# Performance work log

Hardware: AMD Instinct MI355X
Metric: run time of the kernel (lower is better)

## Reference

```python
import jax, jax.numpy as jnp
import numpy as np

TOP_K = 8
NUM_EXPERTS = 64


def setup_inputs() -> dict:
    key = jax.random.key(0)
    k1, k2 = jax.random.split(key)
    x = jax.random.normal(k1, (4, 4096, 2048), dtype=jnp.float32)
    # nn.Linear weight [num_experts, d_model], scaled like typical init
    gate_w = jax.random.normal(k2, (NUM_EXPERTS, 2048), dtype=jnp.float32) * 0.02
    expert_bias = jnp.zeros((NUM_EXPERTS,), dtype=jnp.float32)
    return {"x": x, "gate_w": gate_w, "expert_bias": expert_bias}


def reference(x, gate_w, expert_bias):
    # logits = gate(x): [b, s, E]
    logits = jnp.einsum("bsd,ed->bse", x, gate_w)
    # bias is detached in the original (routing-only, no grad)
    logits_with_bias = logits + jax.lax.stop_gradient(expert_bias)
    # top-k over experts
    top_k_logits, top_k_indices = jax.lax.top_k(logits_with_bias, TOP_K)
    # softmax over the small top-k dimension
    top_k_scores = jax.nn.softmax(top_k_logits, axis=-1)
    # scatter-add load counts per expert (training branch)
    flat_indices = top_k_indices.reshape(-1)
    expert_counts = jnp.zeros((NUM_EXPERTS,), dtype=jnp.int32).at[flat_indices].add(1)
    return top_k_scores, top_k_indices, expert_counts
```

## Files before the change

### kernel.cpp

```cpp
#include <hip/hip_runtime.h>
#include <math.h>

#define DIM   2048
#define NEXP  64
#define TOPK  8
#define BM    32
#define NT    512
#define NBLK  512
#define RSTRIDE 260
#define BUF1  (32 * RSTRIDE)

typedef __attribute__((ext_vector_type(8)))  short bf16x8;
typedef __attribute__((ext_vector_type(16))) float f32x16;

#define MFMA(A, B, C) __builtin_amdgcn_mfma_f32_32x32x16_bf16(A, B, C, 0, 0, 0)
#define AS_BF(v) (*(const bf16x8*)&(v))

#define STR2(x) #x
#define STR(x) STR2(x)
#define GL16(dst, p, off) \
    asm volatile("global_load_dwordx4 %0, %1, off offset:" STR(off) \
                 : "=v"(dst) : "v"(p) : "memory")

__device__ inline unsigned int bfpack(float a, float b) {
    unsigned int ua = __float_as_uint(a), ub = __float_as_uint(b);
    unsigned int lo = (ua + 0x7FFFu + ((ua >> 16) & 1u)) >> 16;
    unsigned int hi = (ub + 0x7FFFu + ((ub >> 16) & 1u)) & 0xFFFF0000u;
    return hi | lo;
}
__device__ inline void split2pair(float a, float b, unsigned int& h, unsigned int& m) {
    h = bfpack(a, b);
    float ra = a - __uint_as_float(h << 16);
    float rb = b - __uint_as_float(h & 0xFFFF0000u);
    m = bfpack(ra, rb);
}

__global__ __launch_bounds__(256) void prep_kernel(const float* __restrict__ w,
                                                   unsigned int* __restrict__ wpack) {
    const int u = blockIdx.x * 256 + threadIdx.x;
    const int e = u >> 8, k8 = u & 255;
    const float4 v0 = *(const float4*)(w + (size_t)e * DIM + k8 * 8);
    const float4 v1 = *(const float4*)(w + (size_t)e * DIM + k8 * 8 + 4);
    unsigned int h[4], m[4];
    split2pair(v0.x, v0.y, h[0], m[0]);
    split2pair(v0.z, v0.w, h[1], m[1]);
    split2pair(v1.x, v1.y, h[2], m[2]);
    split2pair(v1.z, v1.w, h[3], m[3]);
    const int wv = k8 >> 5, t = (k8 >> 1) & 15, kh = k8 & 1;
    const int eh = e >> 5, le = e & 31;
    char* base = (char*)wpack + (size_t)wv * 65536 + t * 4096
               + (eh * 2) * 1024 + (kh * 32 + le) * 16;
    *(uint4*)(base)        = (uint4){h[0], h[1], h[2], h[3]};
    *(uint4*)(base + 1024) = (uint4){m[0], m[1], m[2], m[3]};
}

__global__ __launch_bounds__(NT, 4) void router_kernel(
    const float* __restrict__ x,
    const unsigned int* __restrict__ wpack,
    const float* __restrict__ bias,
    float* __restrict__ out,
    int* __restrict__ histws,
    int M)
{
    __shared__ __align__(16) char smem[67584 + 256];
    float* smemf = (float*)smem;
    int* hist = (int*)(smem + 67584);

    const int tid  = threadIdx.x;
    const int bid  = blockIdx.x;
    const int swz  = (bid & 7) * (NBLK / 8) + (bid >> 3);
    const int row0 = swz * BM;
    if (tid < NEXP) hist[tid] = 0;

    const int wv   = tid >> 6;
    const int lane = tid & 63;
    const int lr   = lane & 31;
    const int kh   = lane >> 5;

    const int xr0 = 4 * wv;
    const float* xsrc0 = x + (size_t)(row0 + xr0 + 0) * DIM + lane * 4;
    const float* xsrc1 = x + (size_t)(row0 + xr0 + 1) * DIM + lane * 4;
    const float* xsrc2 = x + (size_t)(row0 + xr0 + 2) * DIM + lane * 4;
    const float* xsrc3 = x + (size_t)(row0 + xr0 + 3) * DIM + lane * 4;
    const int xo0 = (xr0 + 0) * RSTRIDE + (lane << 2);
    const int xo1 = (xr0 + 1) * RSTRIDE + (lane << 2);
    const int xo2 = (xr0 + 2) * RSTRIDE + (lane << 2);
    const int xo3 = (xr0 + 3) * RSTRIDE + (lane << 2);

    const char* wbase = (const char*)wpack + (2 * wv) * 4096 + lane * 16;

    const int g00 = 8 * wv + 2 * kh;
    const int a00 = lr * RSTRIDE + g00 * 4;
    const int a10 = a00 + 16;

    f32x16 acc0 = {}, acc1 = {};
    uint4 xr0_, xr1_, xr2_, xr3_;
    uint4 w0h_, w0m_, w0H_, w0M_, w1h_, w1m_, w1H_, w1M_;

#define XLD(PH) do { \
        GL16(xr0_, xsrc0 + (PH) * 256, 0); \
        GL16(xr1_, xsrc1 + (PH) * 256, 0); \
        GL16(xr2_, xsrc2 + (PH) * 256, 0); \
        GL16(xr3_, xsrc3 + (PH) * 256, 0); \
    } while (0)

#define WLD(PH) do { \
        const char* a_ = wbase + (PH) * 65536; \
        const char* b_ = a_ + 4096; \
        GL16(w0h_, a_, 0);    GL16(w0m_, a_, 1024); \
        GL16(w0H_, a_, 2048); GL16(w0M_, a_, 3072); \
        GL16(w1h_, b_, 0);    GL16(w1m_, b_, 1024); \
        GL16(w1H_, b_, 2048); GL16(w1M_, b_, 3072); \
    } while (0)

#define DSW(BUFO) do { \
        *(uint4*)(smemf + (BUFO) + xo0) = xr0_; \
        *(uint4*)(smemf + (BUFO) + xo1) = xr1_; \
        *(uint4*)(smemf + (BUFO) + xo2) = xr2_; \
        *(uint4*)(smemf + (BUFO) + xo3) = xr3_; \
    } while (0)

#define DOSPLIT(vlo, vhi, hv, mv) do { \
        unsigned int h_[4], m_[4]; \
        split2pair((vlo).x, (vlo).y, h_[0], m_[0]); \
        split2pair((vlo).z, (vlo).w, h_[1], m_[1]); \
        split2pair((vhi).x, (vhi).y, h_[2], m_[2]); \
        split2pair((vhi).z, (vhi).w, h_[3], m_[3]); \
        hv = (uint4){h_[0], h_[1], h_[2], h_[3]}; \
        mv = (uint4){m_[0], m_[1], m_[2], m_[3]}; \
    } while (0)

#define COMPUTE(BUFO) do { \
        float4 alo0_ = *(const float4*)(smemf + (BUFO) + a00); \
        float4 ahi0_ = *(const float4*)(smemf + (BUFO) + a00 + 4); \
        float4 alo1_ = *(const float4*)(smemf + (BUFO) + a10); \
        float4 ahi1_ = *(const float4*)(smemf + (BUFO) + a10 + 4); \
        uint4 ah_, am_; \
        DOSPLIT(alo0_, ahi0_, ah_, am_); \
        acc0 = MFMA(AS_BF(ah_), AS_BF(w0h_), acc0); \
        acc0 = MFMA(AS_BF(am_), AS_BF(w0h_), acc0); \
        acc0 = MFMA(AS_BF(ah_), AS_BF(w0m_), acc0); \
        acc1 = MFMA(AS_BF(ah_), AS_BF(w0H_), acc1); \
        acc1 = MFMA(AS_BF(am_), AS_BF(w0H_), acc1); \
        acc1 = MFMA(AS_BF(ah_), AS_BF(w0M_), acc1); \
        DOSPLIT(alo1_, ahi1_, ah_, am_); \
        acc0 = MFMA(AS_BF(ah_), AS_BF(w1h_), acc0); \
        acc0 = MFMA(AS_BF(am_), AS_BF(w1h_), acc0); \
        acc0 = MFMA(AS_BF(ah_), AS_BF(w1m_), acc0); \
        acc1 = MFMA(AS_BF(ah_), AS_BF(w1H_), acc1); \
        acc1 = MFMA(AS_BF(am_), AS_BF(w1H_), acc1); \
        acc1 = MFMA(AS_BF(ah_), AS_BF(w1M_), acc1); \
    } while (0)

#define VMW(N) do { asm volatile("s_waitcnt vmcnt(" STR(N) ")" ::: "memory"); \
                    __builtin_amdgcn_sched_barrier(0); } while (0)
#define LGK0 asm volatile("s_waitcnt lgkmcnt(0)" ::: "memory")
#define BAR __builtin_amdgcn_s_barrier()

    XLD(0); WLD(0);
    VMW(8);
    DSW(0); LGK0; BAR;

    XLD(1); VMW(4); COMPUTE(0);    WLD(1); VMW(8); DSW(BUF1); LGK0; BAR;
    XLD(2); VMW(4); COMPUTE(BUF1); WLD(2); VMW(8); DSW(0);    LGK0; BAR;
    XLD(3); VMW(4); COMPUTE(0);    WLD(3); VMW(8); DSW(BUF1); LGK0; BAR;
    XLD(4); VMW(4); COMPUTE(BUF1); WLD(4); VMW(8); DSW(0);    LGK0; BAR;
    XLD(5); VMW(4); COMPUTE(0);    WLD(5); VMW(8); DSW(BUF1); LGK0; BAR;
    XLD(6); VMW(4); COMPUTE(BUF1); WLD(6); VMW(8); DSW(0);    LGK0; BAR;
    XLD(7); VMW(4); COMPUTE(0);    WLD(7); VMW(8); DSW(BUF1); LGK0; BAR;
    VMW(0); COMPUTE(BUF1);

#undef VMW
#undef LGK0
#undef COMPUTE
#undef DOSPLIT
#undef DSW
#undef WLD
#undef XLD

    __syncthreads();

    float* lgf = smemf;
    #pragma unroll
    for (int r = 0; r < 16; ++r) {
        const int rr = (r & 3) + 8 * (r >> 2) + 4 * kh;
        lgf[(wv * 32 + rr) * 66 + lr]      = acc0[r];
        lgf[(wv * 32 + rr) * 66 + 32 + lr] = acc1[r];
    }
    __syncthreads();

    float* out_scores = out;
    float* out_idx    = out + (size_t)M * TOPK;

    #pragma unroll
    for (int i = 0; i < 4; ++i) {
        const int row = wv * 4 + i;
        float vm = bias[lane];
        #pragma unroll
        for (int p = 0; p < 8; ++p) vm += lgf[(p * 32 + row) * 66 + lane];

        float vals[TOPK];
        int   ids[TOPK];
        #pragma unroll
        for (int k = 0; k < TOPK; ++k) {
            float mv = vm;
            int   mi = lane;
            #pragma unroll
            for (int off = 32; off > 0; off >>= 1) {
                float ov = __shfl_xor(mv, off);
                int   oi = __shfl_xor(mi, off);
                if (ov > mv || (ov == mv && oi < mi)) { mv = ov; mi = oi; }
            }
            vals[k] = mv; ids[k] = mi;
            if (lane == mi) { vm = -INFINITY; atomicAdd(&hist[mi], 1); }
        }
        if (lane == 0) {
            const float m = vals[0];
            float e[TOPK];
            float ssum = 0.f;
            #pragma unroll
            for (int k = 0; k < TOPK; ++k) { e[k] = expf(vals[k] - m); ssum += e[k]; }
            const float inv = 1.0f / ssum;
            const size_t base = (size_t)(row0 + row) * TOPK;
            #pragma unroll
            for (int k = 0; k < TOPK; ++k) {
                out_scores[base + k] = e[k] * inv;
                out_idx[base + k]    = (float)ids[k];
            }
        }
    }

    __syncthreads();
    if (tid < NEXP) histws[bid * NEXP + tid] = hist[tid];
}

__global__ __launch_bounds__(512) void reduce_kernel(const int* __restrict__ histws,
                                                     float* __restrict__ counts) {
    __shared__ int partl[8][NEXP];
    const int t = threadIdx.x;
    const int e = t & 63, c = t >> 6;
    int sm = 0;
    for (int b = c; b < NBLK; b += 8) sm += histws[b * NEXP + e];
    partl[c][e] = sm;
    __syncthreads();
    if (t < NEXP) {
        int tot = 0;
        #pragma unroll
        for (int i = 0; i < 8; ++i) tot += partl[i][t];
        counts[t] = (float)tot;
    }
}

extern "C" void kernel_launch(void* const* d_in, const int* in_sizes, int n_in,
                              void* d_out, int out_size, void* d_ws, size_t ws_size,
                              hipStream_t stream) {
    const float* x    = (const float*)d_in[0];
    const float* w    = (const float*)d_in[1];
    const float* bias = (const float*)d_in[2];
    float* out = (float*)d_out;
    const int M = in_sizes[0] / DIM;

    unsigned int* wpack = (unsigned int*)d_ws;
    int* histws = (int*)((char*)d_ws + (1u << 20));
    float* out_counts = out + (size_t)2 * M * TOPK;

    prep_kernel<<<64, 256, 0, stream>>>(w, wpack);
    router_kernel<<<NBLK, NT, 0, stream>>>(x, wpack, bias, out, histws, M);
    reduce_kernel<<<1, 512, 0, stream>>>(histws, out_counts);
}
```

Baseline: 69.02 us.

## Double row tile to 64 per block and serialize cross-wave logit reduction

Each block now handles 64 rows instead of 32, with half as many blocks. Each wave covers a K slice for both 32-row halves, so every weight fragment loaded from global feeds two MFMA accumulators, halving weight traffic per row. The K phase is narrowed to 128 so the staging buffers fit, at the cost of twice as many pipeline phases and barriers. The per-wave partial logits are now summed through shared memory in eight sequential steps with a barrier after each, which adds serialization and keeps fewer blocks per CU busy.

```diff
diff --git a/kernel.cpp b/kernel.cpp
--- a/kernel.cpp
+++ b/kernel.cpp
@@ -4,11 +4,11 @@
 #define DIM   2048
 #define NEXP  64
 #define TOPK  8
-#define BM    32
+#define BM    64
 #define NT    512
-#define NBLK  512
-#define RSTRIDE 260
-#define BUF1  (32 * RSTRIDE)
+#define NBLK  256
+#define RSTRIDE 132
+#define BUF1  (BM * RSTRIDE)
 
 typedef __attribute__((ext_vector_type(8)))  short bf16x8;
 typedef __attribute__((ext_vector_type(16))) float f32x16;
@@ -77,40 +77,37 @@
     const int lr   = lane & 31;
     const int kh   = lane >> 5;
 
-    const int xr0 = 4 * wv;
-    const float* xsrc0 = x + (size_t)(row0 + xr0 + 0) * DIM + lane * 4;
-    const float* xsrc1 = x + (size_t)(row0 + xr0 + 1) * DIM + lane * 4;
-    const float* xsrc2 = x + (size_t)(row0 + xr0 + 2) * DIM + lane * 4;
-    const float* xsrc3 = x + (size_t)(row0 + xr0 + 3) * DIM + lane * 4;
-    const int xo0 = (xr0 + 0) * RSTRIDE + (lane << 2);
-    const int xo1 = (xr0 + 1) * RSTRIDE + (lane << 2);
-    const int xo2 = (xr0 + 2) * RSTRIDE + (lane << 2);
-    const int xo3 = (xr0 + 3) * RSTRIDE + (lane << 2);
-
-    const char* wbase = (const char*)wpack + (2 * wv) * 4096 + lane * 16;
-
-    const int g00 = 8 * wv + 2 * kh;
-    const int a00 = lr * RSTRIDE + g00 * 4;
-    const int a10 = a00 + 16;
-
-    f32x16 acc0 = {}, acc1 = {};
+    const int l5  = lane >> 5;
+    const int xr0 = 8 * wv;
+    const float* xsrc0 = x + (size_t)(row0 + xr0 + 0 + l5) * DIM + lr * 4;
+    const float* xsrc1 = x + (size_t)(row0 + xr0 + 2 + l5) * DIM + lr * 4;
+    const float* xsrc2 = x + (size_t)(row0 + xr0 + 4 + l5) * DIM + lr * 4;
+    const float* xsrc3 = x + (size_t)(row0 + xr0 + 6 + l5) * DIM + lr * 4;
+    const int xo0 = (xr0 + 0 + l5) * RSTRIDE + lr * 4;
+    const int xo1 = (xr0 + 2 + l5) * RSTRIDE + lr * 4;
+    const int xo2 = (xr0 + 4 + l5) * RSTRIDE + lr * 4;
+    const int xo3 = (xr0 + 6 + l5) * RSTRIDE + lr * 4;
+
+    const char* wtb = (const char*)wpack + wv * 4096 + lane * 16;
+
+    const int a0 = lr * RSTRIDE + wv * 16 + kh * 8;
+    const int a1 = (32 + lr) * RSTRIDE + wv * 16 + kh * 8;
+
+    f32x16 acc00 = {}, acc01 = {}, acc10 = {}, acc11 = {};
     uint4 xr0_, xr1_, xr2_, xr3_;
-    uint4 w0h_, w0m_, w0H_, w0M_, w1h_, w1m_, w1H_, w1M_;
+    uint4 w0h_, w0m_, w1h_, w1m_;
 
 #define XLD(PH) do { \
-        GL16(xr0_, xsrc0 + (PH) * 256, 0); \
-        GL16(xr1_, xsrc1 + (PH) * 256, 0); \
-        GL16(xr2_, xsrc2 + (PH) * 256, 0); \
-        GL16(xr3_, xsrc3 + (PH) * 256, 0); \
+        GL16(xr0_, xsrc0 + (PH) * 128, 0); \
+        GL16(xr1_, xsrc1 + (PH) * 128, 0); \
+        GL16(xr2_, xsrc2 + (PH) * 128, 0); \
+        GL16(xr3_, xsrc3 + (PH) * 128, 0); \
     } while (0)
 
 #define WLD(PH) do { \
-        const char* a_ = wbase + (PH) * 65536; \
-        const char* b_ = a_ + 4096; \
-        GL16(w0h_, a_, 0);    GL16(w0m_, a_, 1024); \
-        GL16(w0H_, a_, 2048); GL16(w0M_, a_, 3072); \
-        GL16(w1h_, b_, 0);    GL16(w1m_, b_, 1024); \
-        GL16(w1H_, b_, 2048); GL16(w1M_, b_, 3072); \
+        const char* p_ = wtb + ((PH) >> 1) * 65536 + ((PH) & 1) * 32768; \
+        GL16(w0h_, p_, 0);    GL16(w0m_, p_, 1024); \
+        GL16(w1h_, p_, 2048); GL16(w1m_, p_, 3072); \
     } while (0)
 
 #define DSW(BUFO) do { \
@@ -131,25 +128,25 @@
     } while (0)
 
 #define COMPUTE(BUFO) do { \
-        float4 alo0_ = *(const float4*)(smemf + (BUFO) + a00); \
-        float4 ahi0_ = *(const float4*)(smemf + (BUFO) + a00 + 4); \
-        float4 alo1_ = *(const float4*)(smemf + (BUFO) + a10); \
-        float4 ahi1_ = *(const float4*)(smemf + (BUFO) + a10 + 4); \
+        float4 alo0_ = *(const float4*)(smemf + (BUFO) + a0); \
+        float4 ahi0_ = *(const float4*)(smemf + (BUFO) + a0 + 4); \
+        float4 alo1_ = *(const float4*)(smemf + (BUFO) + a1); \
+        float4 ahi1_ = *(const float4*)(smemf + (BUFO) + a1 + 4); \
         uint4 ah_, am_; \
         DOSPLIT(alo0_, ahi0_, ah_, am_); \
-        acc0 = MFMA(AS_BF(ah_), AS_BF(w0h_), acc0); \
-        acc0 = MFMA(AS_BF(am_), AS_BF(w0h_), acc0); \
-        acc0 = MFMA(AS_BF(ah_), AS_BF(w0m_), acc0); \
-        acc1 = MFMA(AS_BF(ah_), AS_BF(w0H_), acc1); \
-        acc1 = MFMA(AS_BF(am_), AS_BF(w0H_), acc1); \
-        acc1 = MFMA(AS_BF(ah_), AS_BF(w0M_), acc1); \
+        acc00 = MFMA(AS_BF(ah_), AS_BF(w0h_), acc00); \
+        acc00 = MFMA(AS_BF(am_), AS_BF(w0h_), acc00); \
+        acc00 = MFMA(AS_BF(ah_), AS_BF(w0m_), acc00); \
+        acc01 = MFMA(AS_BF(ah_), AS_BF(w1h_), acc01); \
+        acc01 = MFMA(AS_BF(am_), AS_BF(w1h_), acc01); \
+        acc01 = MFMA(AS_BF(ah_), AS_BF(w1m_), acc01); \
         DOSPLIT(alo1_, ahi1_, ah_, am_); \
-        acc0 = MFMA(AS_BF(ah_), AS_BF(w1h_), acc0); \
-        acc0 = MFMA(AS_BF(am_), AS_BF(w1h_), acc0); \
-        acc0 = MFMA(AS_BF(ah_), AS_BF(w1m_), acc0); \
-        acc1 = MFMA(AS_BF(ah_), AS_BF(w1H_), acc1); \
-        acc1 = MFMA(AS_BF(am_), AS_BF(w1H_), acc1); \
-        acc1 = MFMA(AS_BF(ah_), AS_BF(w1M_), acc1); \
+        acc10 = MFMA(AS_BF(ah_), AS_BF(w0h_), acc10); \
+        acc10 = MFMA(AS_BF(am_), AS_BF(w0h_), acc10); \
+        acc10 = MFMA(AS_BF(ah_), AS_BF(w0m_), acc10); \
+        acc11 = MFMA(AS_BF(ah_), AS_BF(w1h_), acc11); \
+        acc11 = MFMA(AS_BF(am_), AS_BF(w1h_), acc11); \
+        acc11 = MFMA(AS_BF(ah_), AS_BF(w1m_), acc11); \
     } while (0)
 
 #define VMW(N) do { asm volatile("s_waitcnt vmcnt(" STR(N) ")" ::: "memory"); \
@@ -157,19 +154,33 @@
 #define LGK0 asm volatile("s_waitcnt lgkmcnt(0)" ::: "memory")
 #define BAR __builtin_amdgcn_s_barrier()
 
+#define PHASE(P, BUFC, BUFN) do { \
+        XLD((P) + 1); VMW(4); COMPUTE(BUFC); WLD((P) + 1); VMW(4); \
+        DSW(BUFN); LGK0; BAR; \
+    } while (0)
+
     XLD(0); WLD(0);
-    VMW(8);
+    VMW(4);
     DSW(0); LGK0; BAR;
 
-    XLD(1); VMW(4); COMPUTE(0);    WLD(1); VMW(8); DSW(BUF1); LGK0; BAR;
-    XLD(2); VMW(4); COMPUTE(BUF1); WLD(2); VMW(8); DSW(0);    LGK0; BAR;
-    XLD(3); VMW(4); COMPUTE(0);    WLD(3); VMW(8); DSW(BUF1); LGK0; BAR;
-    XLD(4); VMW(4); COMPUTE(BUF1); WLD(4); VMW(8); DSW(0);    LGK0; BAR;
-    XLD(5); VMW(4); COMPUTE(0);    WLD(5); VMW(8); DSW(BUF1); LGK0; BAR;
-    XLD(6); VMW(4); COMPUTE(BUF1); WLD(6); VMW(8); DSW(0);    LGK0; BAR;
-    XLD(7); VMW(4); COMPUTE(0);    WLD(7); VMW(8); DSW(BUF1); LGK0; BAR;
+    PHASE( 0, 0,    BUF1);
+    PHASE( 1, BUF1, 0);
+    PHASE( 2, 0,    BUF1);
+    PHASE( 3, BUF1, 0);
+    PHASE( 4, 0,    BUF1);
+    PHASE( 5, BUF1, 0);
+    PHASE( 6, 0,    BUF1);
+    PHASE( 7, BUF1, 0);
+    PHASE( 8, 0,    BUF1);
+    PHASE( 9, BUF1, 0);
+    PHASE(10, 0,    BUF1);
+    PHASE(11, BUF1, 0);
+    PHASE(12, 0,    BUF1);
+    PHASE(13, BUF1, 0);
+    PHASE(14, 0,    BUF1);
     VMW(0); COMPUTE(BUF1);
 
+#undef PHASE
 #undef VMW
 #undef LGK0
 #undef COMPUTE
@@ -180,25 +191,34 @@
 
     __syncthreads();
 
-    float* lgf = smemf;
-    #pragma unroll
-    for (int r = 0; r < 16; ++r) {
-        const int rr = (r & 3) + 8 * (r >> 2) + 4 * kh;
-        lgf[(wv * 32 + rr) * 66 + lr]      = acc0[r];
-        lgf[(wv * 32 + rr) * 66 + 32 + lr] = acc1[r];
+    float* lg = smemf;
+    for (int p = 0; p < 8; ++p) {
+        if (wv == p) {
+            #pragma unroll
+            for (int r = 0; r < 16; ++r) {
+                const int rr = (r & 3) + 8 * (r >> 2) + 4 * kh;
+                if (p == 0) {
+                    lg[rr * 66 + lr]             = acc00[r];
+                    lg[rr * 66 + 32 + lr]        = acc01[r];
+                    lg[(32 + rr) * 66 + lr]      = acc10[r];
+                    lg[(32 + rr) * 66 + 32 + lr] = acc11[r];
+                } else {
+                    lg[rr * 66 + lr]             += acc00[r];
+                    lg[rr * 66 + 32 + lr]        += acc01[r];
+                    lg[(32 + rr) * 66 + lr]      += acc10[r];
+                    lg[(32 + rr) * 66 + 32 + lr] += acc11[r];
+                }
+            }
+        }
+        __syncthreads();
     }
-    __syncthreads();
 
     float* out_scores = out;
     float* out_idx    = out + (size_t)M * TOPK;
 
-    #pragma unroll
-    for (int i = 0; i < 4; ++i) {
-        const int row = wv * 4 + i;
-        float vm = bias[lane];
-        #pragma unroll
-        for (int p = 0; p < 8; ++p) vm += lgf[(p * 32 + row) * 66 + lane];
-
+    for (int r8 = 0; r8 < 8; ++r8) {
+        const int row = wv * 8 + r8;
+        float vm = lg[row * 66 + lane] + bias[lane];
         float vals[TOPK];
         int   ids[TOPK];
         #pragma unroll
```

Measured after the change: 82.24 us. +19.2%, slower.
